# Optimization experiments

Measured on AMD Instinct MI355X. Metric: run time of the kernel, lower is better.

Reference implementation:

```python
import jax, jax.numpy as jnp
import numpy as np

N, S, C, K, V = 8, 8192, 1, 1024, 64  # batch, samples, n_channels, n_classes, vec_len


def setup_inputs() -> dict:
    key = jax.random.key(0)
    k1, k2 = jax.random.split(key)
    x0 = jax.random.normal(k1, (N, S, C, V), dtype=jnp.float32)
    embedding0 = jax.random.normal(k2, (C, K, V), dtype=jnp.float32) * 0.001
    return {"x0": x0, "embedding0": embedding0}


def reference(x0, embedding0):
    # normalize=False path of the original module
    x = x0
    emb = embedding0
    Ns = x.shape[0] * x.shape[1]
    xf = x.reshape(Ns, C, V)  # (Ns, C, V)
    # squared distances ||x - e||^2 without materializing (Ns, C, K, V)
    d2 = (
        jnp.sum(xf * xf, axis=-1)[:, :, None]
        - 2.0 * jnp.einsum("ncv,ckv->nck", xf, emb)
        + jnp.sum(emb * emb, axis=-1)[None, :, :]
    )
    index = jnp.argmin(d2, axis=2)  # (Ns, C); argmin of dist == argmin of dist^2
    # histogram entropy (matches torch histc over bins 0..K-1, divided by len(index)=Ns)
    counts = jnp.zeros((K,), jnp.float32).at[index.reshape(-1)].add(1.0)
    prob = counts / Ns
    safe_log = jnp.log(jnp.where(counts > 0, prob, 1.0))
    entropy = -jnp.sum(jnp.where(counts > 0, prob * safe_log, 0.0))
    # gather codewords: embedding[c, index[n,c]]
    output = emb[jnp.arange(C)[None, :], index].reshape(x.shape)
    out0 = jax.lax.stop_gradient(output - x) + x  # straight-through
    out1 = jnp.sum((jax.lax.stop_gradient(x) - output) ** 2, axis=-1)  # (N,S,C)
    out2 = jnp.sum((x - jax.lax.stop_gradient(output)) ** 2, axis=-1)  # (N,S,C)
    return (out0, out1, out2, entropy)
```

## Files before the change

kernel.cpp:

```cpp
#include <hip/hip_runtime.h>
#include <math.h>

#define NS   65536
#define KK   1024
#define VV   64
#define SPB  128
#define NB   (NS / SPB)
#define CHC  128
#define NCHK (KK / CHC)
#define TPC  (CHC / 16)

#define OUT0_OFF 0
#define OUT1_OFF 4194304
#define OUT2_OFF 4259840
#define ENT_OFF  4325376


typedef __attribute__((ext_vector_type(8))) short bf16x8;
typedef __attribute__((ext_vector_type(4))) float f32x4;

__device__ __forceinline__ short f2bf(float f) {
    unsigned u = __float_as_uint(f);
    u = (u + 0x7fffu + ((u >> 16) & 1u)) >> 16;
    return (short)u;
}

__global__ void vq_prep(const float* __restrict__ emb, unsigned int* __restrict__ hist,
                        float* __restrict__ cinit, short* __restrict__ cb,
                        unsigned int* __restrict__ entCnt) {
    int t = blockIdx.x * blockDim.x + threadIdx.x;
    if (t == 0) entCnt[0] = 0u;
    if (t < KK) {
        hist[t] = 0u;
        const float4* e4 = (const float4*)(emb + (size_t)t * VV);
        float s = 0.f;
        union { short sh[8]; bf16x8 v; } pk;
        bf16x8* dst = (bf16x8*)(cb + (size_t)t * VV);
        #pragma unroll
        for (int i = 0; i < 8; ++i) {
            float4 f0 = e4[2 * i], f1 = e4[2 * i + 1];
            s = fmaf(f0.x, f0.x, s); s = fmaf(f0.y, f0.y, s);
            s = fmaf(f0.z, f0.z, s); s = fmaf(f0.w, f0.w, s);
            s = fmaf(f1.x, f1.x, s); s = fmaf(f1.y, f1.y, s);
            s = fmaf(f1.z, f1.z, s); s = fmaf(f1.w, f1.w, s);
            pk.sh[0] = f2bf(f0.x); pk.sh[1] = f2bf(f0.y);
            pk.sh[2] = f2bf(f0.z); pk.sh[3] = f2bf(f0.w);
            pk.sh[4] = f2bf(f1.x); pk.sh[5] = f2bf(f1.y);
            pk.sh[6] = f2bf(f1.z); pk.sh[7] = f2bf(f1.w);
            dst[i] = pk.v;
        }
        cinit[t] = 1.0f - 0.5f * s;
    }
}

__global__ __launch_bounds__(256, 2) void vq_main(
    const float* __restrict__ x, const float* __restrict__ emb,
    const float* __restrict__ cinit, const short* __restrict__ cb,
    unsigned int* __restrict__ hist,
    float* __restrict__ out0, float* __restrict__ out1, float* __restrict__ out2,
    float* __restrict__ entOut)
{
    __shared__ __align__(16) char  sCB[2][CHC * 128];
    __shared__ __align__(16) float sCI[KK];
    __shared__ unsigned sPk[SPB];
    __shared__ float    sXn[SPB];
    __shared__ float    sPart[4];
    __shared__ unsigned sLast;

    const int tid  = threadIdx.x;
    const int lane = tid & 63;
    const int wv   = tid >> 6;
    const int col  = lane & 15;
    const int quad = lane >> 4;
    const int samp0 = blockIdx.x * SPB;
    const int wbase = wv * 32;

    bf16x8 a[4];
    float  xn[2];
    #pragma unroll
    for (int mt = 0; mt < 2; ++mt) {
        const float* xp = x + (size_t)(samp0 + wbase + mt * 16 + col) * VV + quad * 8;
        float4 p0 = *(const float4*)(xp);
        float4 p1 = *(const float4*)(xp + 4);
        float4 p2 = *(const float4*)(xp + 32);
        float4 p3 = *(const float4*)(xp + 36);
        bf16x8 lo, hi;
        lo[0]=f2bf(p0.x); lo[1]=f2bf(p0.y); lo[2]=f2bf(p0.z); lo[3]=f2bf(p0.w);
        lo[4]=f2bf(p1.x); lo[5]=f2bf(p1.y); lo[6]=f2bf(p1.z); lo[7]=f2bf(p1.w);
        hi[0]=f2bf(p2.x); hi[1]=f2bf(p2.y); hi[2]=f2bf(p2.z); hi[3]=f2bf(p2.w);
        hi[4]=f2bf(p3.x); hi[5]=f2bf(p3.y); hi[6]=f2bf(p3.z); hi[7]=f2bf(p3.w);
        a[2 * mt] = lo; a[2 * mt + 1] = hi;
        float s = 0.f;
        s=fmaf(p0.x,p0.x,s); s=fmaf(p0.y,p0.y,s); s=fmaf(p0.z,p0.z,s); s=fmaf(p0.w,p0.w,s);
        s=fmaf(p1.x,p1.x,s); s=fmaf(p1.y,p1.y,s); s=fmaf(p1.z,p1.z,s); s=fmaf(p1.w,p1.w,s);
        s=fmaf(p2.x,p2.x,s); s=fmaf(p2.y,p2.y,s); s=fmaf(p2.z,p2.z,s); s=fmaf(p2.w,p2.w,s);
        s=fmaf(p3.x,p3.x,s); s=fmaf(p3.y,p3.y,s); s=fmaf(p3.z,p3.z,s); s=fmaf(p3.w,p3.w,s);
        xn[mt] = s;
    }
    #pragma unroll
    for (int mt = 0; mt < 2; ++mt) {
        xn[mt] += __shfl_xor(xn[mt], 16, 64);
        xn[mt] += __shfl_xor(xn[mt], 32, 64);
    }

    ((float4*)sCI)[tid] = ((const float4*)cinit)[tid];
    int woff[4];
    #pragma unroll
    for (int i = 0; i < 4; ++i) {
        int gid = i * 256 + tid;
        int c = gid >> 3, g = gid & 7;
        woff[i] = c * 128 + ((g ^ (c & 7)) << 4);
    }
    {
        const float4* g0 = (const float4*)cb;
        #pragma unroll
        for (int i = 0; i < 4; ++i)
            *(float4*)(sCB[0] + woff[i]) = g0[i * 256 + tid];
    }
    __syncthreads();

    unsigned pm[8];
    #pragma unroll
    for (int j = 0; j < 8; ++j) pm[j] = 0u;

    const int rb0off = col * 128 + ((quad ^ (col & 7)) << 4);
    const int rb1off = col * 128 + (((4 + quad) ^ (col & 7)) << 4);
    const unsigned invc = 1023u - (unsigned)col;

    for (int ch = 0; ch < NCHK; ++ch) {
        float4 pf[4];
        if (ch < NCHK - 1) {
            const float4* g = (const float4*)(cb + (size_t)(ch + 1) * CHC * VV);
            #pragma unroll
            for (int i = 0; i < 4; ++i) pf[i] = g[i * 256 + tid];
        }
        const char* B = sCB[ch & 1];
        const unsigned invch = invc - (unsigned)(ch * CHC);
        #pragma unroll
        for (int tl = 0; tl < TPC; ++tl) {
            bf16x8 b0 = *(const bf16x8*)(B + tl * 2048 + rb0off);
            bf16x8 b1 = *(const bf16x8*)(B + tl * 2048 + rb1off);
            float ci = sCI[ch * CHC + tl * 16 + col];
            f32x4 cv = {ci, ci, ci, ci};
            const unsigned inv = invch - (unsigned)(tl * 16);
            #pragma unroll
            for (int mt = 0; mt < 2; ++mt) {
                f32x4 acc = __builtin_amdgcn_mfma_f32_16x16x32_bf16(a[2*mt],     b0, cv,  0, 0, 0);
                acc       = __builtin_amdgcn_mfma_f32_16x16x32_bf16(a[2*mt + 1], b1, acc, 0, 0, 0);
                #pragma unroll
                for (int r = 0; r < 4; ++r) {
                    unsigned pk2 = (__float_as_uint(acc[r]) & 0xFFFFFC00u) | inv;
                    pm[mt*4+r] = (pk2 > pm[mt*4+r]) ? pk2 : pm[mt*4+r];
                }
            }
        }
        if (ch < NCHK - 1) {
            char* dstB = sCB[(ch + 1) & 1];
            #pragma unroll
            for (int i = 0; i < 4; ++i) *(float4*)(dstB + woff[i]) = pf[i];
        }
        __syncthreads();
    }

    #pragma unroll
    for (int off = 1; off < 16; off <<= 1) {
        #pragma unroll
        for (int j = 0; j < 8; ++j) {
            unsigned o = (unsigned)__shfl_xor((int)pm[j], off, 64);
            pm[j] = (o > pm[j]) ? o : pm[j];
        }
    }
    if (col == 0) {
        #pragma unroll
        for (int mt = 0; mt < 2; ++mt)
            #pragma unroll
            for (int r = 0; r < 4; ++r)
                sPk[wbase + mt * 16 + quad * 4 + r] = pm[mt * 4 + r];
    }
    if (quad == 0) {
        #pragma unroll
        for (int mt = 0; mt < 2; ++mt) sXn[wbase + mt * 16 + col] = xn[mt];
    }
    __syncthreads();

    if (tid < SPB) {
        unsigned p = sPk[tid];
        int   code = 1023 - (int)(p & 1023u);
        float sf   = __uint_as_float(p & 0xFFFFFC00u);
        float d    = fmaf(-2.f, sf - 1.0f, sXn[tid]);
        int n = samp0 + tid;
        out1[n] = d;
        out2[n] = d;
        atomicAdd(&hist[code], 1u);
    }
    {
        const int smp  = tid >> 1;
        const int half = tid & 1;
        const int code = 1023 - (int)(sPk[smp] & 1023u);
        const float4* src = (const float4*)(emb + (size_t)code * VV + half * 32);
        float4*       dst = (float4*)(out0 + (size_t)(samp0 + smp) * VV + half * 32);
        #pragma unroll
        for (int i = 0; i < 8; ++i) dst[i] = src[i];
    }

    __syncthreads();
    unsigned int* entCnt = (unsigned int*)entOut;
    if (tid == 0) sLast = (atomicAdd(entCnt, 1u) == (NB - 1)) ? 1u : 0u;
    __syncthreads();
    if (sLast) {
        float e = 0.f;
        #pragma unroll
        for (int i = 0; i < 4; ++i) {
            unsigned c = atomicAdd(&hist[i * 256 + tid], 0u);
            if (c) { float p = (float)c * (1.0f / (float)NS); e -= p * logf(p); }
        }
        #pragma unroll
        for (int off = 32; off > 0; off >>= 1) e += __shfl_down(e, off, 64);
        if (lane == 0) sPart[wv] = e;
        __syncthreads();
        if (tid == 0) entOut[0] = sPart[0] + sPart[1] + sPart[2] + sPart[3];
    }
}

extern "C" void kernel_launch(void* const* d_in, const int* in_sizes, int n_in,
                              void* d_out, int out_size, void* d_ws, size_t ws_size,
                              hipStream_t stream) {
    const float* x   = (const float*)d_in[0];
    const float* emb = (const float*)d_in[1];
    float* out = (float*)d_out;
    unsigned int* hist  = (unsigned int*)d_ws;
    float*        cinit = (float*)((char*)d_ws + 4096);
    short*        cb    = (short*)((char*)d_ws + 8192);

    vq_prep<<<4, 256, 0, stream>>>(emb, hist, cinit, cb, (unsigned int*)(out + ENT_OFF));
    vq_main<<<NB, 256, 0, stream>>>(x, emb, cinit, cb, hist,
                                    out + OUT0_OFF, out + OUT1_OFF, out + OUT2_OFF,
                                    out + ENT_OFF);
}
```

Before: 109.7 us.

## Stream codebook chunks straight into LDS asynchronously, double chunk size, pair max reductions

The prep kernel now writes the bf16 codebook in a pre-swizzled layout, so the main kernel can copy chunks from global memory straight into LDS with global_load_lds. This replaces the earlier path of loading into registers and then storing to shared memory. The codebook chunk grows from 128 to 256 codes, which halves the number of loop iterations and barriers. The running argmax update now merges two tiles before touching the accumulator, which is meant to allow 3-input max instructions and cut VALU work. The trade-off is double the LDS footprint, which pressures occupancy, and a dependence on barriers correctly waiting for the async LDS loads to finish.

New measurement: 101.3 us. -7.6%, faster.

```diff
diff --git a/kernel.cpp b/kernel.cpp
--- a/kernel.cpp
+++ b/kernel.cpp
@@ -6,9 +6,10 @@
 #define VV   64
 #define SPB  128
 #define NB   (NS / SPB)
-#define CHC  128
+#define CHC  256
 #define NCHK (KK / CHC)
 #define TPC  (CHC / 16)
+#define CHB  (CHC * VV * 2)
 
 #define OUT0_OFF 0
 #define OUT1_OFF 4194304
@@ -18,6 +19,10 @@
 
 typedef __attribute__((ext_vector_type(8))) short bf16x8;
 typedef __attribute__((ext_vector_type(4))) float f32x4;
+
+#define ASYNC16(gp, lp) __builtin_amdgcn_global_load_lds(                      \
+    (const __attribute__((address_space(1))) unsigned int*)(gp),               \
+    (__attribute__((address_space(3))) unsigned int*)(lp), 16, 0, 0)
 
 __device__ __forceinline__ short f2bf(float f) {
     unsigned u = __float_as_uint(f);
@@ -33,12 +38,13 @@
     if (t < KK) {
         hist[t] = 0u;
         const float4* e4 = (const float4*)(emb + (size_t)t * VV);
+        const int ch = t >> 8, cw = t & 255;
+        short* base = cb + (size_t)ch * (CHC * VV) + cw * 64;
         float s = 0.f;
         union { short sh[8]; bf16x8 v; } pk;
-        bf16x8* dst = (bf16x8*)(cb + (size_t)t * VV);
-        #pragma unroll
-        for (int i = 0; i < 8; ++i) {
-            float4 f0 = e4[2 * i], f1 = e4[2 * i + 1];
+        #pragma unroll
+        for (int g = 0; g < 8; ++g) {
+            float4 f0 = e4[2 * g], f1 = e4[2 * g + 1];
             s = fmaf(f0.x, f0.x, s); s = fmaf(f0.y, f0.y, s);
             s = fmaf(f0.z, f0.z, s); s = fmaf(f0.w, f0.w, s);
             s = fmaf(f1.x, f1.x, s); s = fmaf(f1.y, f1.y, s);
@@ -47,7 +53,7 @@
             pk.sh[2] = f2bf(f0.z); pk.sh[3] = f2bf(f0.w);
             pk.sh[4] = f2bf(f1.x); pk.sh[5] = f2bf(f1.y);
             pk.sh[6] = f2bf(f1.z); pk.sh[7] = f2bf(f1.w);
-            dst[i] = pk.v;
+            *(bf16x8*)(base + ((g ^ (cw & 7)) * 8)) = pk.v;
         }
         cinit[t] = 1.0f - 0.5f * s;
     }
@@ -60,7 +66,7 @@
     float* __restrict__ out0, float* __restrict__ out1, float* __restrict__ out2,
     float* __restrict__ entOut)
 {
-    __shared__ __align__(16) char  sCB[2][CHC * 128];
+    __shared__ __align__(16) char  sCB[2][CHB];
     __shared__ __align__(16) float sCI[KK];
     __shared__ unsigned sPk[SPB];
     __shared__ float    sXn[SPB];
@@ -74,6 +80,16 @@
     const int quad = lane >> 4;
     const int samp0 = blockIdx.x * SPB;
     const int wbase = wv * 32;
+
+    {
+        const char* g0 = (const char*)cb;
+        #pragma unroll
+        for (int i = 0; i < 8; ++i) {
+            const int off = (i * 256 + tid) * 16;
+            ASYNC16(g0 + off, sCB[0] + off);
+        }
+        ((float4*)sCI)[tid] = ((const float4*)cinit)[tid];
+    }
 
     bf16x8 a[4];
     float  xn[2];
@@ -102,21 +118,6 @@
         xn[mt] += __shfl_xor(xn[mt], 16, 64);
         xn[mt] += __shfl_xor(xn[mt], 32, 64);
     }
-
-    ((float4*)sCI)[tid] = ((const float4*)cinit)[tid];
-    int woff[4];
-    #pragma unroll
-    for (int i = 0; i < 4; ++i) {
-        int gid = i * 256 + tid;
-        int c = gid >> 3, g = gid & 7;
-        woff[i] = c * 128 + ((g ^ (c & 7)) << 4);
-    }
-    {
-        const float4* g0 = (const float4*)cb;
-        #pragma unroll
-        for (int i = 0; i < 4; ++i)
-            *(float4*)(sCB[0] + woff[i]) = g0[i * 256 + tid];
-    }
     __syncthreads();
 
     unsigned pm[8];
@@ -128,14 +129,18 @@
     const unsigned invc = 1023u - (unsigned)col;
 
     for (int ch = 0; ch < NCHK; ++ch) {
-        float4 pf[4];
-        if (ch < NCHK - 1) {
-            const float4* g = (const float4*)(cb + (size_t)(ch + 1) * CHC * VV);
+        if (ch + 1 < NCHK) {
+            const char* g = (const char*)cb + (size_t)(ch + 1) * CHB;
+            char* nb = sCB[(ch + 1) & 1];
             #pragma unroll
-            for (int i = 0; i < 4; ++i) pf[i] = g[i * 256 + tid];
+            for (int i = 0; i < 8; ++i) {
+                const int off = (i * 256 + tid) * 16;
+                ASYNC16(g + off, nb + off);
+            }
         }
         const char* B = sCB[ch & 1];
         const unsigned invch = invc - (unsigned)(ch * CHC);
+        unsigned pkp[8];
         #pragma unroll
         for (int tl = 0; tl < TPC; ++tl) {
             bf16x8 b0 = *(const bf16x8*)(B + tl * 2048 + rb0off);
@@ -143,21 +148,25 @@
             float ci = sCI[ch * CHC + tl * 16 + col];
             f32x4 cv = {ci, ci, ci, ci};
             const unsigned inv = invch - (unsigned)(tl * 16);
+            unsigned pk2[8];
             #pragma unroll
             for (int mt = 0; mt < 2; ++mt) {
                 f32x4 acc = __builtin_amdgcn_mfma_f32_16x16x32_bf16(a[2*mt],     b0, cv,  0, 0, 0);
                 acc       = __builtin_amdgcn_mfma_f32_16x16x32_bf16(a[2*mt + 1], b1, acc, 0, 0, 0);
                 #pragma unroll
-                for (int r = 0; r < 4; ++r) {
-                    unsigned pk2 = (__float_as_uint(acc[r]) & 0xFFFFFC00u) | inv;
-                    pm[mt*4+r] = (pk2 > pm[mt*4+r]) ? pk2 : pm[mt*4+r];
+                for (int r = 0; r < 4; ++r)
+                    pk2[mt*4+r] = (__float_as_uint(acc[r]) & 0xFFFFFC00u) | inv;
+            }
+            if (tl & 1) {
+                #pragma unroll
+                for (int j = 0; j < 8; ++j) {
+                    unsigned t2 = pkp[j] > pk2[j] ? pkp[j] : pk2[j];
+                    pm[j] = pm[j] > t2 ? pm[j] : t2;
                 }
+            } else {
+                #pragma unroll
+                for (int j = 0; j < 8; ++j) pkp[j] = pk2[j];
             }
-        }
-        if (ch < NCHK - 1) {
-            char* dstB = sCB[(ch + 1) & 1];
-            #pragma unroll
-            for (int i = 0; i < 4; ++i) *(float4*)(dstB + woff[i]) = pf[i];
         }
         __syncthreads();
     }
```
